# Kernel optimization log

Hardware: AMD Instinct MI355X
Metric: run time of the kernel (lower is better)

Reference implementation:

```python
import jax, jax.numpy as jnp
import numpy as np

B, D, C, T, DEPTH = 4096, 1024, 1000, 32, 6
N_INTERNAL = 2 ** DEPTH - 1
N_LEAVES = 2 ** DEPTH


def setup_inputs() -> dict:
    key = jax.random.key(0)
    k0, k1, k2 = jax.random.split(key, 3)
    x = jax.random.normal(k0, (B, D), jnp.float32)
    split_weights = jax.random.normal(k1, (T, N_INTERNAL, D), jnp.float32) * 0.1
    split_biases = jnp.zeros((T, N_INTERNAL), jnp.float32)
    leaf_logits = jax.random.normal(k2, (T, N_LEAVES, C), jnp.float32) * 0.1
    tree_weights = jnp.ones((T,), jnp.float32) / T
    log_temperature = jnp.zeros((), jnp.float32)
    return {
        "x": x,
        "split_weights": split_weights,
        "split_biases": split_biases,
        "leaf_logits": leaf_logits,
        "tree_weights": tree_weights,
        "log_temperature": log_temperature,
    }


def reference(x, split_weights, split_biases, leaf_logits, tree_weights, log_temperature):
    depth = int(np.log2(leaf_logits.shape[1]))
    temp = jnp.clip(jnp.exp(log_temperature), 0.1, 5.0)
    # split probabilities for all trees at once: [B, T, I]
    logits = jnp.einsum('bd,tid->bti', x, split_weights) + split_biases[None, :, :]
    s = jax.nn.sigmoid(logits / temp)
    b, t, _ = s.shape
    # iterative-doubling path probabilities; BFS leaf order matches the
    # original per-leaf loop (left child multiplies (1-s), right multiplies s)
    mu = jnp.ones((b, t, 1), s.dtype)
    for d in range(depth):
        lvl = s[:, :, 2 ** d - 1: 2 ** (d + 1) - 1]  # [B, T, 2^d] level-d splits
        mu = jnp.stack([mu * (1.0 - lvl), mu * lvl], axis=-1).reshape(b, t, 2 ** (d + 1))
    leaf_class_probs = jax.nn.softmax(leaf_logits / temp, axis=-1)  # [T, L, C]
    w = jax.nn.softmax(tree_weights, axis=0)                        # [T]
    # fused tree-weighted blend, avoids materializing [B, T, C]
    return jnp.einsum('btl,t,tlc->bc', mu, w, leaf_class_probs)
```

## Files before the change

kernel.cpp:

```cpp
#include <hip/hip_runtime.h>
#include <cstdint>
#include <cstddef>

constexpr int Bv = 4096;
constexpr int Dv = 1024;
constexpr int Cv = 1000;
constexpr int Tv = 32;
constexpr int NI = 63;
constexpr int NL = 64;
constexpr int TNp = 2048;
constexpr int TL = Tv * NL;
constexpr int Npad = 1024;

typedef _Float16 h8  __attribute__((ext_vector_type(8)));
typedef _Float16 h4  __attribute__((ext_vector_type(4)));
typedef short    s8v __attribute__((ext_vector_type(8)));
typedef unsigned short us8 __attribute__((ext_vector_type(8)));
typedef float    f4v __attribute__((ext_vector_type(4)));

constexpr size_t N_X    = (size_t)Bv * Dv;
constexpr size_t N_W    = (size_t)TNp * Dv;
constexpr size_t OFF_XH = 64;
constexpr size_t OFF_WH = OFF_XH + N_X / 2;
constexpr size_t OFF_P  = OFF_WH + N_W / 2;
constexpr size_t OFF_MH = OFF_P + (size_t)TL * Cv;
constexpr size_t OFF_PTH= OFF_MH + (size_t)Bv * TL / 2;

__device__ __forceinline__ unsigned short f2bf_rn(float x) {
    unsigned u = __float_as_uint(x);
    return (unsigned short)((u + 0x7fffu + ((u >> 16) & 1u)) >> 16);
}

__device__ __forceinline__ void gll16(const void* gptr, void* lptr) {
    __builtin_amdgcn_global_load_lds(
        (const __attribute__((address_space(1))) unsigned int*)gptr,
        (__attribute__((address_space(3))) unsigned int*)lptr,
        16, 0, 0);
}

__global__ __launch_bounds__(256)
void k_prep_leaf(const float* __restrict__ x, const float* __restrict__ sw,
                 const float* __restrict__ ll, const float* __restrict__ lt,
                 _Float16* __restrict__ Xh, _Float16* __restrict__ Wh,
                 float* __restrict__ P) {
    const int b = blockIdx.x;
    const int tid = threadIdx.x;
    if (b < 4096) {
        const size_t i4 = ((size_t)b * 256 + tid) * 4;
        const float4 v = *reinterpret_cast<const float4*>(&x[i4]);
        h4 vh;
        vh[0] = (_Float16)v.x; vh[1] = (_Float16)v.y;
        vh[2] = (_Float16)v.z; vh[3] = (_Float16)v.w;
        *reinterpret_cast<h4*>(&Xh[i4]) = vh;
    } else if (b < 6144) {
        const size_t d4 = ((size_t)(b - 4096) * 256 + tid) * 4;
        const int row = (int)(d4 >> 10);
        const int col = (int)(d4 & 1023);
        const int t = row >> 6, i = row & 63;
        float4 v = make_float4(0.f, 0.f, 0.f, 0.f);
        if (i < NI)
            v = *reinterpret_cast<const float4*>(&sw[(size_t)(t * NI + i) * Dv + col]);
        h4 vh;
        vh[0] = (_Float16)v.x; vh[1] = (_Float16)v.y;
        vh[2] = (_Float16)v.z; vh[3] = (_Float16)v.w;
        *reinterpret_cast<h4*>(&Wh[d4]) = vh;
    } else {
        const int r = b - 6144;
        const float temp = fminf(fmaxf(expf(lt[0]), 0.1f), 5.0f);
        const float invT = 1.0f / temp;
        const float* row = ll + (size_t)r * Cv;
        float* pr = P + (size_t)r * Cv;
        __shared__ float redm[4];
        __shared__ float reds[4];

        float m = -3.4e38f;
        for (int c = tid; c < Cv; c += 256) m = fmaxf(m, row[c] * invT);
        #pragma unroll
        for (int o = 32; o > 0; o >>= 1) m = fmaxf(m, __shfl_down(m, o));
        if ((tid & 63) == 0) redm[tid >> 6] = m;
        __syncthreads();
        m = fmaxf(fmaxf(redm[0], redm[1]), fmaxf(redm[2], redm[3]));

        float sum = 0.f;
        for (int c = tid; c < Cv; c += 256) {
            const float e = expf(row[c] * invT - m);
            pr[c] = e;
            sum += e;
        }
        #pragma unroll
        for (int o = 32; o > 0; o >>= 1) sum += __shfl_down(sum, o);
        if ((tid & 63) == 0) reds[tid >> 6] = sum;
        __syncthreads();
        sum = reds[0] + reds[1] + reds[2] + reds[3];
        const float rs = 1.0f / sum;
        for (int c = tid; c < Cv; c += 256) pr[c] *= rs;
    }
}

__global__ __launch_bounds__(256, 2)
void k_gemm1mu_tp(const _Float16* __restrict__ Xh, const _Float16* __restrict__ Wh,
                  const float* __restrict__ bias, const float* __restrict__ tw,
                  const float* __restrict__ lt, const float* __restrict__ P,
                  unsigned short* __restrict__ MH, unsigned short* __restrict__ PTH) {
    __shared__ __align__(16) char lds[4 * 64 * 65 * 4];

    const int tid = threadIdx.x;

    if (blockIdx.x >= 512) {
        const int tpb = blockIdx.x - 512;
        const int k0 = (tpb & 31) * 64;
        const int c0 = (tpb >> 5) * 64;
        float* T = (float*)lds;
        #pragma unroll
        for (int i = 0; i < 16; ++i) {
            const int idx = tid + i * 256;
            const int kk = idx >> 6, cc = idx & 63;
            const int c = c0 + cc;
            T[kk * 65 + cc] = (c < Cv) ? P[(size_t)(k0 + kk) * Cv + c] : 0.f;
        }
        __syncthreads();
        #pragma unroll
        for (int i = 0; i < 16; ++i) {
            const int idx = tid + i * 256;
            const int cc = idx >> 6, kk = idx & 63;
            PTH[(size_t)(c0 + cc) * TL + k0 + kk] = f2bf_rn(T[kk * 65 + cc]);
        }
        return;
    }

    const int wg  = (blockIdx.x & 7) * 64 + (blockIdx.x >> 3);
    const int blk = wg >> 6;
    const int j   = wg & 63;
    const int bx  = (blk & 3) * 4 + (j & 3);
    const int by  = (blk >> 2) * 16 + (j >> 2);
    const int bm = by * 128, bn = bx * 128;

    const int lane = tid & 63, wv = tid >> 6;
    const int wr = wv >> 1, wc = wv & 1;
    const int lrow = lane & 15, kg = (lane >> 4) * 8;
    const int sr = lane >> 3;
    const int sc = (lane & 7) * 8;

    const float temp = fminf(fmaxf(expf(lt[0]), 0.1f), 5.0f);
    const float invT = 1.0f / temp;
    const int mytree = 2 * bx + wc;
    float wm = -3.4e38f;
    #pragma unroll
    for (int t = 0; t < Tv; ++t) wm = fmaxf(wm, tw[t]);
    float wsum = 0.f, wmine = 0.f;
    #pragma unroll
    for (int t = 0; t < Tv; ++t) {
        const float e = expf(tw[t] - wm);
        wsum += e;
        if (t == mytree) wmine = e;
    }
    const float wt = wmine / wsum;

    f4v acc[4][4] = {};

#define STG(bufi, k0)                                                         \
    { _Pragma("unroll")                                                       \
      for (int i_ = 0; i_ < 4; ++i_) {                                        \
        const int ch_  = wv * 4 + i_;                                         \
        const int row_ = ch_ * 8 + sr;                                        \
        gll16(&Xh[(size_t)(bm + row_) * Dv + (k0) + sc],                      \
              lds + (bufi) * 32768 + ch_ * 1024);                             \
        gll16(&Wh[(size_t)(bn + row_) * Dv + (k0) + sc],                      \
              lds + (bufi) * 32768 + 16384 + ch_ * 1024);                     \
      } }

    STG(0, 0);
    for (int t = 0; t < 16; ++t) {
        const int cur = t & 1;
        if (t < 15) {
            STG(cur ^ 1, (t + 1) * 64);
            asm volatile("s_waitcnt vmcnt(8)" ::: "memory");
        } else {
            asm volatile("s_waitcnt vmcnt(0)" ::: "memory");
        }
        __builtin_amdgcn_s_barrier();
        __builtin_amdgcn_sched_barrier(0);

        #pragma unroll
        for (int kh = 0; kh < 2; ++kh) {
            h8 a[4], b[4];
            #pragma unroll
            for (int mf = 0; mf < 4; ++mf)
                a[mf] = *reinterpret_cast<const h8*>(
                    lds + cur * 32768 + ((wr * 64 + mf * 16 + lrow) * 64 + kh * 32 + kg) * 2);
            #pragma unroll
            for (int nf = 0; nf < 4; ++nf)
                b[nf] = *reinterpret_cast<const h8*>(
                    lds + cur * 32768 + 16384 + ((wc * 64 + nf * 16 + lrow) * 64 + kh * 32 + kg) * 2);
            #pragma unroll
            for (int mf = 0; mf < 4; ++mf)
                #pragma unroll
                for (int nf = 0; nf < 4; ++nf)
                    acc[mf][nf] = __builtin_amdgcn_mfma_f32_16x16x32_f16(a[mf], b[nf], acc[mf][nf], 0, 0, 0);
        }

        __builtin_amdgcn_sched_barrier(0);
        asm volatile("s_waitcnt lgkmcnt(0)" ::: "memory");
        __builtin_amdgcn_s_barrier();
    }
#undef STG

    float* scr = (float*)lds + wv * (64 * 65);
    #pragma unroll
    for (int nf = 0; nf < 4; ++nf) {
        const int colB = nf * 16 + lrow;
        const int gcol = bn + wc * 64 + colB;
        const int ii = gcol & 63;
        const float bv = (ii < NI) ? bias[(gcol >> 6) * NI + ii] : 0.f;
        #pragma unroll
        for (int mf = 0; mf < 4; ++mf) {
            #pragma unroll
            for (int r = 0; r < 4; ++r) {
                const int rowB = mf * 16 + (lane >> 4) * 4 + r;
                const float z = (acc[mf][nf][r] + bv) * invT;
                scr[rowB * 65 + colB] = 1.0f / (1.0f + __expf(-z));
            }
        }
    }
    asm volatile("s_waitcnt lgkmcnt(0)" ::: "memory");

    const float* srow = scr + lane * 65;
    float mu[NL];
    mu[0] = wt;
    #pragma unroll
    for (int d = 0; d < 6; ++d) {
        const int width = 1 << d;
        #pragma unroll
        for (int i = width - 1; i >= 0; --i) {
            const float sv = srow[width - 1 + i];
            const float m  = mu[i];
            mu[2 * i + 1] = m * sv;
            mu[2 * i]     = m * (1.0f - sv);
        }
    }
    const size_t obase = (size_t)(bm + wr * 64 + lane) * TL + (size_t)mytree * 64;
    #pragma unroll
    for (int c = 0; c < 8; ++c) {
        us8 vh;
        #pragma unroll
        for (int jj = 0; jj < 8; ++jj) vh[jj] = f2bf_rn(mu[c * 8 + jj]);
        *reinterpret_cast<us8*>(&MH[obase + c * 8]) = vh;
    }
}

__global__ __launch_bounds__(256, 2)
void k_gemm2(const unsigned short* __restrict__ MH, const unsigned short* __restrict__ PTH,
             float* __restrict__ out) {
    __shared__ unsigned short LA[2][2][128][32];
    __shared__ unsigned short LB[2][2][64][32];

    const int tid  = threadIdx.x;
    const int wg  = (blockIdx.x & 7) * 64 + (blockIdx.x >> 3);
    const int blk = wg >> 6;
    const int j   = wg & 63;
    const int bnt = (blk & 1) * 8 + (j & 7);
    const int bmt = (blk >> 1) * 8 + (j >> 3);
    const int bm = bmt * 128, bn = bnt * 64;

    const int lane = tid & 63;
    const int wv   = tid >> 6;
    const int wr   = wv >> 1;
    const int wc   = wv & 1;
    const int lrow = lane & 15;
    const int kg   = (lane >> 4) * 8;
    const int sr   = lane >> 2;
    const int sc   = (lane & 3) * 8;

    f4v acc[4][2] = {};

#define STAGE2(bufi, k0)                                                          \
    { _Pragma("unroll")                                                           \
      for (int kh_ = 0; kh_ < 2; ++kh_) {                                         \
        _Pragma("unroll")                                                         \
        for (int i_ = 0; i_ < 2; ++i_) {                                          \
          const int ch_  = wv * 2 + i_;                                           \
          const int row_ = ch_ * 16 + sr;                                         \
          gll16(&MH[(size_t)(bm + row_) * TL + (k0) + kh_ * 32 + sc],             \
                (char*)&LA[bufi][kh_][0][0] + ch_ * 1024);                        \
        }                                                                         \
        { const int row_ = wv * 16 + sr;                                          \
          gll16(&PTH[(size_t)(bn + row_) * TL + (k0) + kh_ * 32 + sc],            \
                (char*)&LB[bufi][kh_][0][0] + wv * 1024); }                       \
      } }

    STAGE2(0, 0);
    for (int t = 0; t < 32; ++t) {
        const int cur = t & 1;
        if (t < 31) {
            STAGE2(cur ^ 1, (t + 1) * 64);
            asm volatile("s_waitcnt vmcnt(6)" ::: "memory");
        } else {
            asm volatile("s_waitcnt vmcnt(0)" ::: "memory");
        }
        __builtin_amdgcn_s_barrier();
        __builtin_amdgcn_sched_barrier(0);

        #pragma unroll
        for (int kh = 0; kh < 2; ++kh) {
            s8v a[4], b[2];
            #pragma unroll
            for (int mf = 0; mf < 4; ++mf)
                a[mf] = *reinterpret_cast<const s8v*>(&LA[cur][kh][wr * 64 + mf * 16 + lrow][kg]);
            #pragma unroll
            for (int nf = 0; nf < 2; ++nf)
                b[nf] = *reinterpret_cast<const s8v*>(&LB[cur][kh][wc * 32 + nf * 16 + lrow][kg]);
            #pragma unroll
            for (int mf = 0; mf < 4; ++mf)
                #pragma unroll
                for (int nf = 0; nf < 2; ++nf)
                    acc[mf][nf] = __builtin_amdgcn_mfma_f32_16x16x32_bf16(a[mf], b[nf], acc[mf][nf], 0, 0, 0);
        }

        __builtin_amdgcn_sched_barrier(0);
        asm volatile("s_waitcnt lgkmcnt(0)" ::: "memory");
        __builtin_amdgcn_s_barrier();
    }
#undef STAGE2

    #pragma unroll
    for (int nf = 0; nf < 2; ++nf) {
        const int col = bn + wc * 32 + nf * 16 + lrow;
        if (col >= Cv) continue;
        #pragma unroll
        for (int mf = 0; mf < 4; ++mf) {
            #pragma unroll
            for (int r = 0; r < 4; ++r) {
                const int row = bm + wr * 64 + mf * 16 + (lane >> 4) * 4 + r;
                out[(size_t)row * Cv + col] = acc[mf][nf][r];
            }
        }
    }
}

extern "C" void kernel_launch(void* const* d_in, const int* in_sizes, int n_in,
                              void* d_out, int out_size, void* d_ws, size_t ws_size,
                              hipStream_t stream) {
    const float* x  = (const float*)d_in[0];
    const float* sw = (const float*)d_in[1];
    const float* sb = (const float*)d_in[2];
    const float* ll = (const float*)d_in[3];
    const float* tw = (const float*)d_in[4];
    const float* lt = (const float*)d_in[5];

    float* out  = (float*)d_out;
    float* ws   = (float*)d_ws;
    _Float16* Xh = (_Float16*)(ws + OFF_XH);
    _Float16* Wh = (_Float16*)(ws + OFF_WH);
    float* Pbuf = ws + OFF_P;
    unsigned short* MH  = (unsigned short*)(ws + OFF_MH);
    unsigned short* PTH = (unsigned short*)(ws + OFF_PTH);

    k_prep_leaf<<<8192, 256, 0, stream>>>(x, sw, ll, lt, Xh, Wh, Pbuf);
    k_gemm1mu_tp<<<1024, 256, 0, stream>>>(Xh, Wh, sb, tw, lt, Pbuf, MH, PTH);
    k_gemm2<<<512, 256, 0, stream>>>(MH, PTH, out);
}
```

Before: 85.83 us.

## Load GEMM B-operand fragments directly from global into registers, bypassing LDS

In both GEMM kernels the B operand (split weights in gemm1, leaf probs in gemm2) is now read straight from global memory into double-buffered register fragments instead of being staged through LDS. Only the A tile stays in LDS, which halves LDS traffic and footprint. gemm2 is also reshaped to 128 threads, each wave covering 64x64. The aim is to cut LDS bandwidth and barrier cost, at the price of more registers, possibly lower occupancy, and uncoalesced per-lane global B loads that wait on vmcnt.

```diff
diff --git a/kernel.cpp b/kernel.cpp
--- a/kernel.cpp
+++ b/kernel.cpp
@@ -157,53 +157,70 @@
     const float wt = wmine / wsum;
 
     f4v acc[4][4] = {};
-
-#define STG(bufi, k0)                                                         \
+    h8 breg0[4][2], breg1[4][2];
+
+#define STG_A(bufi, k0)                                                       \
     { _Pragma("unroll")                                                       \
       for (int i_ = 0; i_ < 4; ++i_) {                                        \
         const int ch_  = wv * 4 + i_;                                         \
         const int row_ = ch_ * 8 + sr;                                        \
         gll16(&Xh[(size_t)(bm + row_) * Dv + (k0) + sc],                      \
-              lds + (bufi) * 32768 + ch_ * 1024);                             \
-        gll16(&Wh[(size_t)(bn + row_) * Dv + (k0) + sc],                      \
-              lds + (bufi) * 32768 + 16384 + ch_ * 1024);                     \
+              lds + (bufi) * 16384 + ch_ * 1024);                             \
       } }
 
-    STG(0, 0);
-    for (int t = 0; t < 16; ++t) {
-        const int cur = t & 1;
-        if (t < 15) {
-            STG(cur ^ 1, (t + 1) * 64);
-            asm volatile("s_waitcnt vmcnt(8)" ::: "memory");
-        } else {
-            asm volatile("s_waitcnt vmcnt(0)" ::: "memory");
-        }
-        __builtin_amdgcn_s_barrier();
-        __builtin_amdgcn_sched_barrier(0);
-
-        #pragma unroll
-        for (int kh = 0; kh < 2; ++kh) {
-            h8 a[4], b[4];
-            #pragma unroll
-            for (int mf = 0; mf < 4; ++mf)
-                a[mf] = *reinterpret_cast<const h8*>(
-                    lds + cur * 32768 + ((wr * 64 + mf * 16 + lrow) * 64 + kh * 32 + kg) * 2);
-            #pragma unroll
-            for (int nf = 0; nf < 4; ++nf)
-                b[nf] = *reinterpret_cast<const h8*>(
-                    lds + cur * 32768 + 16384 + ((wc * 64 + nf * 16 + lrow) * 64 + kh * 32 + kg) * 2);
-            #pragma unroll
-            for (int mf = 0; mf < 4; ++mf)
-                #pragma unroll
-                for (int nf = 0; nf < 4; ++nf)
-                    acc[mf][nf] = __builtin_amdgcn_mfma_f32_16x16x32_f16(a[mf], b[nf], acc[mf][nf], 0, 0, 0);
-        }
-
-        __builtin_amdgcn_sched_barrier(0);
-        asm volatile("s_waitcnt lgkmcnt(0)" ::: "memory");
-        __builtin_amdgcn_s_barrier();
-    }
-#undef STG
+#define BLOAD1(dst, k0)                                                       \
+    { _Pragma("unroll")                                                       \
+      for (int nf_ = 0; nf_ < 4; ++nf_) {                                     \
+        _Pragma("unroll")                                                     \
+        for (int kh_ = 0; kh_ < 2; ++kh_) {                                   \
+          dst[nf_][kh_] = *reinterpret_cast<const h8*>(                       \
+              &Wh[(size_t)(bn + wc * 64 + nf_ * 16 + lrow) * Dv +             \
+                  (k0) + kh_ * 32 + kg]);                                     \
+        } } }
+
+#define ITER1(T, CBUF, CURB, NBUF, NXTB, LAST)                                \
+  {                                                                           \
+    if (!(LAST)) {                                                            \
+      STG_A(NBUF, ((T) + 1) * 64);                                            \
+      BLOAD1(NXTB, ((T) + 1) * 64);                                           \
+      __builtin_amdgcn_sched_barrier(0);                                      \
+      asm volatile("s_waitcnt vmcnt(12)" ::: "memory");                       \
+    } else {                                                                  \
+      asm volatile("s_waitcnt vmcnt(0)" ::: "memory");                        \
+    }                                                                         \
+    __builtin_amdgcn_s_barrier();                                             \
+    __builtin_amdgcn_sched_barrier(0);                                        \
+    _Pragma("unroll")                                                         \
+    for (int kh = 0; kh < 2; ++kh) {                                          \
+      h8 a_[4];                                                               \
+      _Pragma("unroll")                                                       \
+      for (int mf = 0; mf < 4; ++mf)                                          \
+        a_[mf] = *reinterpret_cast<const h8*>(                                \
+            lds + (CBUF) * 16384 +                                            \
+            ((wr * 64 + mf * 16 + lrow) * 64 + kh * 32 + kg) * 2);            \
+      _Pragma("unroll")                                                       \
+      for (int mf = 0; mf < 4; ++mf)                                          \
+        _Pragma("unroll")                                                     \
+        for (int nf = 0; nf < 4; ++nf)                                        \
+          acc[mf][nf] = __builtin_amdgcn_mfma_f32_16x16x32_f16(               \
+              a_[mf], CURB[nf][kh], acc[mf][nf], 0, 0, 0);                    \
+    }                                                                         \
+    __builtin_amdgcn_sched_barrier(0);                                        \
+    asm volatile("s_waitcnt lgkmcnt(0)" ::: "memory");                        \
+    __builtin_amdgcn_s_barrier();                                             \
+  }
+
+    STG_A(0, 0);
+    BLOAD1(breg0, 0);
+    for (int tt = 0; tt < 7; ++tt) {
+        ITER1(2 * tt,     0, breg0, 1, breg1, false);
+        ITER1(2 * tt + 1, 1, breg1, 0, breg0, false);
+    }
+    ITER1(14, 0, breg0, 1, breg1, false);
+    ITER1(15, 1, breg1, 0, breg0, true);
+#undef ITER1
+#undef BLOAD1
+#undef STG_A
 
     float* scr = (float*)lds + wv * (64 * 65);
     #pragma unroll
@@ -248,11 +265,10 @@
     }
 }
 
-__global__ __launch_bounds__(256, 2)
+__global__ __launch_bounds__(128, 2)
 void k_gemm2(const unsigned short* __restrict__ MH, const unsigned short* __restrict__ PTH,
              float* __restrict__ out) {
-    __shared__ unsigned short LA[2][2][128][32];
-    __shared__ unsigned short LB[2][2][64][32];
+    __shared__ __align__(16) char lds[2 * 16384];
 
     const int tid  = threadIdx.x;
     const int wg  = (blockIdx.x & 7) * 64 + (blockIdx.x >> 3);
@@ -264,73 +280,86 @@
 
     const int lane = tid & 63;
     const int wv   = tid >> 6;
-    const int wr   = wv >> 1;
-    const int wc   = wv & 1;
     const int lrow = lane & 15;
     const int kg   = (lane >> 4) * 8;
-    const int sr   = lane >> 2;
-    const int sc   = (lane & 3) * 8;
-
-    f4v acc[4][2] = {};
-
-#define STAGE2(bufi, k0)                                                          \
-    { _Pragma("unroll")                                                           \
-      for (int kh_ = 0; kh_ < 2; ++kh_) {                                         \
-        _Pragma("unroll")                                                         \
-        for (int i_ = 0; i_ < 2; ++i_) {                                          \
-          const int ch_  = wv * 2 + i_;                                           \
-          const int row_ = ch_ * 16 + sr;                                         \
-          gll16(&MH[(size_t)(bm + row_) * TL + (k0) + kh_ * 32 + sc],             \
-                (char*)&LA[bufi][kh_][0][0] + ch_ * 1024);                        \
-        }                                                                         \
-        { const int row_ = wv * 16 + sr;                                          \
-          gll16(&PTH[(size_t)(bn + row_) * TL + (k0) + kh_ * 32 + sc],            \
-                (char*)&LB[bufi][kh_][0][0] + wv * 1024); }                       \
+    const int sr   = lane >> 3;
+    const int sc   = (lane & 7) * 8;
+
+    f4v acc[4][4] = {};
+    s8v breg0[4][2], breg1[4][2];
+
+#define STG2(bufi, k0)                                                        \
+    { _Pragma("unroll")                                                       \
+      for (int i_ = 0; i_ < 8; ++i_) {                                        \
+        const int ch_  = wv * 8 + i_;                                         \
+        const int row_ = ch_ * 8 + sr;                                        \
+        gll16(&MH[(size_t)(bm + row_) * TL + (k0) + sc],                      \
+              lds + (bufi) * 16384 + ch_ * 1024);                             \
       } }
 
-    STAGE2(0, 0);
-    for (int t = 0; t < 32; ++t) {
-        const int cur = t & 1;
-        if (t < 31) {
-            STAGE2(cur ^ 1, (t + 1) * 64);
-            asm volatile("s_waitcnt vmcnt(6)" ::: "memory");
-        } else {
-            asm volatile("s_waitcnt vmcnt(0)" ::: "memory");
-        }
-        __builtin_amdgcn_s_barrier();
-        __builtin_amdgcn_sched_barrier(0);
-
-        #pragma unroll
-        for (int kh = 0; kh < 2; ++kh) {
-            s8v a[4], b[2];
-            #pragma unroll
-            for (int mf = 0; mf < 4; ++mf)
-                a[mf] = *reinterpret_cast<const s8v*>(&LA[cur][kh][wr * 64 + mf * 16 + lrow][kg]);
-            #pragma unroll
-            for (int nf = 0; nf < 2; ++nf)
-                b[nf] = *reinterpret_cast<const s8v*>(&LB[cur][kh][wc * 32 + nf * 16 + lrow][kg]);
-            #pragma unroll
-            for (int mf = 0; mf < 4; ++mf)
-                #pragma unroll
-                for (int nf = 0; nf < 2; ++nf)
-                    acc[mf][nf] = __builtin_amdgcn_mfma_f32_16x16x32_bf16(a[mf], b[nf], acc[mf][nf], 0, 0, 0);
-        }
-
-        __builtin_amdgcn_sched_barrier(0);
-        asm volatile("s_waitcnt lgkmcnt(0)" ::: "memory");
-        __builtin_amdgcn_s_barrier();
-    }
-#undef STAGE2
-
-    #pragma unroll
-    for (int nf = 0; nf < 2; ++nf) {
-        const int col = bn + wc * 32 + nf * 16 + lrow;
+#define BLOAD2(dst, k0)                                                       \
+    { _Pragma("unroll")                                                       \
+      for (int nf_ = 0; nf_ < 4; ++nf_) {                                     \
+        _Pragma("unroll")                                                     \
+        for (int kh_ = 0; kh_ < 2; ++kh_) {                                   \
+          dst[nf_][kh_] = *reinterpret_cast<const s8v*>(                      \
+              &PTH[(size_t)(bn + nf_ * 16 + lrow) * TL +                      \
+                   (k0) + kh_ * 32 + kg]);                                    \
+        } } }
+
+#define ITER2(T, CBUF, CURB, NBUF, NXTB, LAST)                                \
+  {                                                                           \
+    if (!(LAST)) {                                                            \
+      STG2(NBUF, ((T) + 1) * 64);                                             \
+      BLOAD2(NXTB, ((T) + 1) * 64);                                           \
+      __builtin_amdgcn_sched_barrier(0);                                      \
+      asm volatile("s_waitcnt vmcnt(16)" ::: "memory");                       \
+    } else {                                                                  \
+      asm volatile("s_waitcnt vmcnt(0)" ::: "memory");                        \
+    }                                                                         \
+    __builtin_amdgcn_s_barrier();                                             \
+    __builtin_amdgcn_sched_barrier(0);                                        \
+    _Pragma("unroll")                                                         \
+    for (int kh = 0; kh < 2; ++kh) {                                          \
+      s8v a_[4];                                                              \
+      _Pragma("unroll")                                                       \
+      for (int mf = 0; mf < 4; ++mf)                                          \
+        a_[mf] = *reinterpret_cast<const s8v*>(                               \
+            lds + (CBUF) * 16384 +                                            \
+            ((wv * 64 + mf * 16 + lrow) * 64 + kh * 32 + kg) * 2);            \
+      _Pragma("unroll")                                                       \
+      for (int mf = 0; mf < 4; ++mf)                                          \
+        _Pragma("unroll")                                                     \
+        for (int nf = 0; nf < 4; ++nf)                                        \
+          acc[mf][nf] = __builtin_amdgcn_mfma_f32_16x16x32_bf16(              \
+              a_[mf], CURB[nf][kh], acc[mf][nf], 0, 0, 0);                    \
+    }                                                                         \
+    __builtin_amdgcn_sched_barrier(0);                                        \
+    asm volatile("s_waitcnt lgkmcnt(0)" ::: "memory");                        \
+    __builtin_amdgcn_s_barrier();                                             \
+  }
+
+    STG2(0, 0);
+    BLOAD2(breg0, 0);
+    for (int tt = 0; tt < 15; ++tt) {
+        ITER2(2 * tt,     0, breg0, 1, breg1, false);
+        ITER2(2 * tt + 1, 1, breg1, 0, breg0, false);
+    }
+    ITER2(30, 0, breg0, 1, breg1, false);
+    ITER2(31, 1, breg1, 0, breg0, true);
+#undef ITER2
+#undef BLOAD2
+#undef STG2
+
+    #pragma unroll
+    for (int nf = 0; nf < 4; ++nf) {
+        const int col = bn + nf * 16 + lrow;
         if (col >= Cv) continue;
         #pragma unroll
         for (int mf = 0; mf < 4; ++mf) {
             #pragma unroll
             for (int r = 0; r < 4; ++r) {
-                const int row = bm + wr * 64 + mf * 16 + (lane >> 4) * 4 + r;
+                const int row = bm + wv * 64 + mf * 16 + (lane >> 4) * 4 + r;
                 out[(size_t)row * Cv + col] = acc[mf][nf][r];
             }
         }
@@ -357,5 +386,5 @@
 
     k_prep_leaf<<<8192, 256, 0, stream>>>(x, sw, ll, lt, Xh, Wh, Pbuf);
     k_gemm1mu_tp<<<1024, 256, 0, stream>>>(Xh, Wh, sb, tw, lt, Pbuf, MH, PTH);
-    k_gemm2<<<512, 256, 0, stream>>>(MH, PTH, out);
-}
+    k_gemm2<<<512, 128, 0, stream>>>(MH, PTH, out);
+}
```

Result: slower. 112.3 us (+30.8%).
